# Optimization experiments

Measured on AMD Instinct MI355X. Metric: run time of the kernel, lower is better.

Reference implementation:

```python
import jax, jax.numpy as jnp
import numpy as np

B, CIN, COUT, K, H, W, STYLE_DIM = 16, 128, 128, 3, 128, 128, 512

def setup_inputs() -> dict:
    key = jax.random.key(0)
    k1, k2, k3, k4 = jax.random.split(key, 4)
    x = jax.random.normal(k1, (B, CIN, H, W), dtype=jnp.float32)
    style = jax.random.normal(k2, (B, STYLE_DIM), dtype=jnp.float32)
    weight = jax.random.normal(k3, (COUT, CIN, K, K), dtype=jnp.float32)
    mod_w = jax.random.normal(k4, (CIN, STYLE_DIM), dtype=jnp.float32)
    mod_b = jnp.ones((CIN,), dtype=jnp.float32)  # EqualLinear bias_init=1
    return {"x": x, "style": style, "weight": weight, "mod_w": mod_w, "mod_b": mod_b}

def reference(x, style, weight, mod_w, mod_b):
    b, cin, h, w = x.shape
    cout, _, k, _ = weight.shape
    scale = 1.0 / np.sqrt(cin * k * k)        # conv equalized-lr scale
    lin_scale = 1.0 / np.sqrt(mod_w.shape[1])  # EqualLinear scale (lr_mul=1)
    pad = k // 2
    # affine modulation: EqualLinear(style_dim -> in_channels), bias_init=1
    s = style @ (mod_w * lin_scale).T + mod_b               # [B, Cin]
    # per-sample modulated weights
    wmod = scale * weight[None] * s[:, None, :, None, None]  # [B, Cout, Cin, k, k]
    demod = jax.lax.rsqrt(jnp.sum(wmod * wmod, axis=(2, 3, 4)) + 1e-8)  # [B, Cout]
    wmod = wmod * demod[:, :, None, None, None]
    # grouped conv with groups=batch == vmapped per-sample conv
    def conv_one(xi, wi):
        return jax.lax.conv_general_dilated(
            xi[None], wi, window_strides=(1, 1), padding=[(pad, pad), (pad, pad)],
            dimension_numbers=("NCHW", "OIHW", "NCHW"))[0]
    out = jax.vmap(conv_one)(x, wmod)  # [B, Cout, H, W]
    return out
```

## Files before the change

kernel.cpp:

```cpp
#include <hip/hip_runtime.h>
#include <hip/hip_bf16.h>


typedef __attribute__((ext_vector_type(8))) short short8;
typedef __attribute__((ext_vector_type(4))) float f32x4;

#define XPITCH (130 * 128)
#define CONV_SCALE 0.029462782549439483f
#define LIN_SCALE 0.04419417382415922f

__device__ __forceinline__ void async16(unsigned short* lds, const unsigned short* g) {
  __builtin_amdgcn_global_load_lds((const __attribute__((address_space(1))) void*)g,
                                   (__attribute__((address_space(3))) void*)lds, 16, 0, 0);
}

__device__ __forceinline__ unsigned int pack2bf(float a, float b) {
  unsigned short ha = __builtin_bit_cast(unsigned short, __float2bfloat16(a));
  unsigned short hb = __builtin_bit_cast(unsigned short, __float2bfloat16(b));
  return (unsigned int)ha | ((unsigned int)hb << 16);
}

__global__ void style_kernel(const float* __restrict__ style, const float* __restrict__ mod_w,
                             const float* __restrict__ mod_b, float* __restrict__ s_ws) {
  const int gw = blockIdx.x * 4 + (threadIdx.x >> 6);
  const int b = gw >> 7, cin = gw & 127, lane = threadIdx.x & 63;
  const float4 s0 = *(const float4*)(style + (size_t)b * 512 + lane * 4);
  const float4 s1 = *(const float4*)(style + (size_t)b * 512 + 256 + lane * 4);
  const float4 w0 = *(const float4*)(mod_w + (size_t)cin * 512 + lane * 4);
  const float4 w1 = *(const float4*)(mod_w + (size_t)cin * 512 + 256 + lane * 4);
  float acc = s0.x * w0.x + s0.y * w0.y + s0.z * w0.z + s0.w * w0.w +
              s1.x * w1.x + s1.y * w1.y + s1.z * w1.z + s1.w * w1.w;
#pragma unroll
  for (int off = 32; off; off >>= 1) acc += __shfl_xor(acc, off);
  if (lane == 0) s_ws[b * 128 + cin] = acc * LIN_SCALE + mod_b[cin];
}

__global__ void modw_kernel(const float* __restrict__ weight, const float* __restrict__ s_ws,
                            unsigned short* __restrict__ w_ws) {
  const int bid = blockIdx.x;
  const int b = bid >> 7, cout = bid & 127;
  const int cin = threadIdx.x;
  const float sv = s_ws[b * 128 + cin] * CONV_SCALE;
  const float* wp = weight + ((size_t)cout * 128 + cin) * 9;
  float v[9];
  float ss = 0.f;
#pragma unroll
  for (int j = 0; j < 9; ++j) { v[j] = wp[j] * sv; ss += v[j] * v[j]; }
#pragma unroll
  for (int off = 32; off; off >>= 1) ss += __shfl_down(ss, off);
  __shared__ float red[2];
  if ((threadIdx.x & 63) == 0) red[threadIdx.x >> 6] = ss;
  __syncthreads();
  const float dem = rsqrtf(red[0] + red[1] + 1e-8f);
#pragma unroll
  for (int j = 0; j < 9; ++j) {
    __hip_bfloat16 h = __float2bfloat16(v[j] * dem);
    w_ws[(((size_t)b * 9 + j) * 128 + cout) * 128 + cin] =
        __builtin_bit_cast(unsigned short, h);
  }
}

__global__ __launch_bounds__(256) void nhwc_kernel(const float* __restrict__ x,
                                                   unsigned short* __restrict__ xp) {
  const int b = blockIdx.y, row = blockIdx.x;
  const int tid = threadIdx.x;
  unsigned short* ob = xp + ((size_t)b * 130 + row) * XPITCH;
  if (row == 0 || row == 129) {
    const uint4 z = {0u, 0u, 0u, 0u};
    for (int v = tid; v < 1040; v += 256) ((uint4*)ob)[v] = z;
    return;
  }
  const int y = row - 1;
  __shared__ unsigned short T[128 * 128];
  const float* xb = x + (size_t)b * (128 * 16384) + y * 128;

  const int xc4 = tid & 31;
  const int cing = tid >> 5;
#pragma unroll
  for (int r = 0; r < 4; ++r) {
    const int cin0 = r * 32 + cing * 4;
    const int g = cin0 >> 2;
    float4 f[4];
#pragma unroll
    for (int j = 0; j < 4; ++j)
      f[j] = *(const float4*)(xb + (size_t)(cin0 + j) * 16384 + xc4 * 4);
#pragma unroll
    for (int i = 0; i < 4; ++i) {
      const int xc = xc4 * 4 + i;
      const int gp = g ^ (xc & 31);
      uint2 col;
      col.x = pack2bf(((const float*)&f[0])[i], ((const float*)&f[1])[i]);
      col.y = pack2bf(((const float*)&f[2])[i], ((const float*)&f[3])[i]);
      *(uint2*)(&T[xc * 128 + gp * 4]) = col;
    }
  }
  __syncthreads();
#pragma unroll
  for (int rr = 0; rr < 8; ++rr) {
    const int v = rr * 256 + tid;
    const int cg = v & 15;
    const int xc = v >> 4;
    const int s5 = xc & 31;
    const int g0 = (cg * 2) ^ s5, g1 = (cg * 2 + 1) ^ s5;
    const uint2 a = *(const uint2*)(&T[xc * 128 + g0 * 4]);
    const uint2 c = *(const uint2*)(&T[xc * 128 + g1 * 4]);
    uint4 o;
    o.x = a.x; o.y = a.y; o.z = c.x; o.w = c.y;
    *(uint4*)(ob + (xc + 1) * 128 + cg * 8) = o;
  }
  const uint4 z = {0u, 0u, 0u, 0u};
  if (tid < 16) *(uint4*)(ob + tid * 8) = z;
  else if (tid < 32) *(uint4*)(ob + 129 * 128 + (tid - 16) * 8) = z;
}

__global__ __launch_bounds__(512, 2) void conv_kernel(const unsigned short* __restrict__ xp,
                                                      const unsigned short* __restrict__ wws,
                                                      float* __restrict__ out) {
  __shared__ unsigned short lA[2][128 * 64];
  __shared__ unsigned short lB[2][256 * 64];

  const int tid = threadIdx.x;
  const int bid = (blockIdx.x & 7) * 128 + (blockIdx.x >> 3);
  const int b = bid >> 6, y0 = (bid & 63) * 2;
  const int lane = tid & 63, w = tid >> 6;
  const int wm = w & 1, wn = w >> 1;
  const int l15 = lane & 15, q = lane >> 4;

  f32x4 acc[4][4];
#pragma unroll
  for (int i = 0; i < 4; ++i)
#pragma unroll
    for (int t = 0; t < 4; ++t) acc[i][t] = (f32x4){0.f, 0.f, 0.f, 0.f};

  const unsigned short* xpb = xp + (size_t)b * 130 * XPITCH;
  const unsigned short* wb = wws + (size_t)b * 9 * 128 * 128;

  const int am = tid >> 3;
  const unsigned short* asrc = wb + am * 128 + (((tid & 7) ^ (am & 7)) << 3);
  const unsigned short* bsrc[4];
#pragma unroll
  for (int p = 0; p < 4; ++p) {
    const int g = p * 512 + tid, n = g >> 3;
    const int c16 = (g & 7) ^ (n & 7);
    bsrc[p] = xpb + (size_t)(y0 + (n >> 7)) * XPITCH + (n & 127) * 128 + (c16 << 3);
  }
  const int dst8 = tid * 8;

#define STAGE_STEP(cur_, j3_, ky_, kx_, c0_)                         \
  do {                                                               \
    const int ka = (j3_) * 16384 + (c0_);                            \
    async16(lA[cur_] + dst8, asrc + ka);                             \
    async16(lA[cur_] + 4096 + dst8, asrc + ka + 8192);               \
    const int kb = (ky_)*XPITCH + (kx_)*128 + (c0_);                 \
    async16(lB[cur_] + dst8, bsrc[0] + kb);                          \
    async16(lB[cur_] + 4096 + dst8, bsrc[1] + kb);                   \
    async16(lB[cur_] + 8192 + dst8, bsrc[2] + kb);                   \
    async16(lB[cur_] + 12288 + dst8, bsrc[3] + kb);                  \
  } while (0)

  STAGE_STEP(0, 0, 0, 0, 0);

#pragma unroll
  for (int t = 0; t < 18; ++t) {
    const int cur = t & 1;
    if (t < 17) {
      const int tn = t + 1;
      const int j3n = tn >> 1, c0n = (tn & 1) << 6;
      const int kyn = j3n / 3, kxn = j3n % 3;
      STAGE_STEP(cur ^ 1, j3n, kyn, kxn, c0n);
      asm volatile("s_waitcnt vmcnt(6)" ::: "memory");
    } else {
      asm volatile("s_waitcnt vmcnt(0)" ::: "memory");
    }
    asm volatile("s_barrier" ::: "memory");

    short8 af[2][4], bf[2][4];
#pragma unroll
    for (int s = 0; s < 2; ++s) {
      const int axor = (((s * 4 + q) ^ (l15 & 7)) << 3);
#pragma unroll
      for (int i = 0; i < 4; ++i)
        af[s][i] = *(const short8*)(&lA[cur][(wm * 64 + i * 16 + l15) * 64 + axor]);
#pragma unroll
      for (int i = 0; i < 4; ++i)
        bf[s][i] = *(const short8*)(&lB[cur][(wn * 64 + i * 16 + l15) * 64 + axor]);
    }
    asm volatile("s_waitcnt lgkmcnt(0)" ::: "memory");
    __builtin_amdgcn_sched_barrier(0);
    __builtin_amdgcn_s_setprio(1);
#pragma unroll
    for (int s = 0; s < 2; ++s)
#pragma unroll
      for (int i = 0; i < 4; ++i)
#pragma unroll
        for (int u = 0; u < 4; ++u)
          acc[i][u] = __builtin_amdgcn_mfma_f32_16x16x32_bf16(af[s][i], bf[s][u], acc[i][u], 0, 0, 0);
    __builtin_amdgcn_s_setprio(0);
    asm volatile("s_barrier" ::: "memory");
  }
#undef STAGE_STEP

  float* obase = out + (size_t)b * (128 * 16384) + (y0 + (wn >> 1)) * 128 + (wn & 1) * 64;
#pragma unroll
  for (int i = 0; i < 4; ++i) {
    const int coutb = wm * 64 + i * 16 + q * 4;
#pragma unroll
    for (int rr = 0; rr < 4; ++rr) {
      float* orow = obase + (size_t)(coutb + rr) * 16384;
#pragma unroll
      for (int t = 0; t < 4; ++t) orow[t * 16 + l15] = acc[i][t][rr];
    }
  }
}

extern "C" void kernel_launch(void* const* d_in, const int* in_sizes, int n_in,
                              void* d_out, int out_size, void* d_ws, size_t ws_size,
                              hipStream_t stream) {
  const float* x = (const float*)d_in[0];
  const float* style = (const float*)d_in[1];
  const float* weight = (const float*)d_in[2];
  const float* mod_w = (const float*)d_in[3];
  const float* mod_b = (const float*)d_in[4];
  float* out = (float*)d_out;

  char* ws = (char*)d_ws;
  float* s_ws = (float*)ws;
  unsigned short* w_ws = (unsigned short*)(ws + 8192);
  unsigned short* xp = (unsigned short*)(ws + (5u << 20));

  style_kernel<<<512, 256, 0, stream>>>(style, mod_w, mod_b, s_ws);
  modw_kernel<<<16 * 128, 128, 0, stream>>>(weight, s_ws, w_ws);
  nhwc_kernel<<<dim3(130, 16), 256, 0, stream>>>(x, xp);
  conv_kernel<<<16 * 64, 512, 0, stream>>>(xp, w_ws, out);
}
```

Before: 348.1 us.

## Fold style modulation into input and demod into output epilogue; triple-buffer conv

Instead of building a modulated bf16 weight tensor per sample, the style scale is applied to the input during the NHWC bf16 conversion. A single shared bf16 weight tensor is used by all samples, and demodulation is computed from precomputed squared weight sums and applied as a per-output-channel scale in the conv epilogue. This removes the per-batch weight generation and makes weight loads shared across blocks, which is friendlier to L2. The conv main loop is also restructured into 36 smaller K-steps of 32 channels with a three-stage LDS pipeline. Rounding behaviour changes because bf16 quantisation now happens on the modulated activations rather than on the modulated weights.

```diff
diff --git a/kernel.cpp b/kernel.cpp
--- a/kernel.cpp
+++ b/kernel.cpp
@@ -35,32 +35,35 @@
   if (lane == 0) s_ws[b * 128 + cin] = acc * LIN_SCALE + mod_b[cin];
 }
 
-__global__ void modw_kernel(const float* __restrict__ weight, const float* __restrict__ s_ws,
-                            unsigned short* __restrict__ w_ws) {
-  const int bid = blockIdx.x;
-  const int b = bid >> 7, cout = bid & 127;
-  const int cin = threadIdx.x;
-  const float sv = s_ws[b * 128 + cin] * CONV_SCALE;
+__global__ void wprep_kernel(const float* __restrict__ weight,
+                             unsigned short* __restrict__ wsh, float* __restrict__ W2) {
+  const int cout = blockIdx.x, cin = threadIdx.x;
   const float* wp = weight + ((size_t)cout * 128 + cin) * 9;
-  float v[9];
   float ss = 0.f;
 #pragma unroll
-  for (int j = 0; j < 9; ++j) { v[j] = wp[j] * sv; ss += v[j] * v[j]; }
-#pragma unroll
-  for (int off = 32; off; off >>= 1) ss += __shfl_down(ss, off);
-  __shared__ float red[2];
-  if ((threadIdx.x & 63) == 0) red[threadIdx.x >> 6] = ss;
-  __syncthreads();
-  const float dem = rsqrtf(red[0] + red[1] + 1e-8f);
-#pragma unroll
   for (int j = 0; j < 9; ++j) {
-    __hip_bfloat16 h = __float2bfloat16(v[j] * dem);
-    w_ws[(((size_t)b * 9 + j) * 128 + cout) * 128 + cin] =
-        __builtin_bit_cast(unsigned short, h);
-  }
+    const float v = wp[j] * CONV_SCALE;
+    ss += v * v;
+    wsh[j * 16384 + cout * 128 + cin] =
+        __builtin_bit_cast(unsigned short, __float2bfloat16(v));
+  }
+  W2[cout * 128 + cin] = ss;
+}
+
+__global__ void demod_kernel(const float* __restrict__ W2, const float* __restrict__ s_ws,
+                             float* __restrict__ d_ws) {
+  const int gw = blockIdx.x * 4 + (threadIdx.x >> 6);
+  const int b = gw >> 7, cout = gw & 127, lane = threadIdx.x & 63;
+  const float2 w2 = *(const float2*)(W2 + cout * 128 + lane * 2);
+  const float2 sv = *(const float2*)(s_ws + b * 128 + lane * 2);
+  float acc = w2.x * sv.x * sv.x + w2.y * sv.y * sv.y;
+#pragma unroll
+  for (int off = 32; off; off >>= 1) acc += __shfl_xor(acc, off);
+  if (lane == 0) d_ws[b * 128 + cout] = rsqrtf(acc + 1e-8f);
 }
 
 __global__ __launch_bounds__(256) void nhwc_kernel(const float* __restrict__ x,
+                                                   const float* __restrict__ s_ws,
                                                    unsigned short* __restrict__ xp) {
   const int b = blockIdx.y, row = blockIdx.x;
   const int tid = threadIdx.x;
@@ -80,10 +83,14 @@
   for (int r = 0; r < 4; ++r) {
     const int cin0 = r * 32 + cing * 4;
     const int g = cin0 >> 2;
+    const float4 sv = *(const float4*)(s_ws + b * 128 + cin0);
     float4 f[4];
 #pragma unroll
-    for (int j = 0; j < 4; ++j)
+    for (int j = 0; j < 4; ++j) {
       f[j] = *(const float4*)(xb + (size_t)(cin0 + j) * 16384 + xc4 * 4);
+      const float s = ((const float*)&sv)[j];
+      f[j].x *= s; f[j].y *= s; f[j].z *= s; f[j].w *= s;
+    }
 #pragma unroll
     for (int i = 0; i < 4; ++i) {
       const int xc = xc4 * 4 + i;
@@ -114,10 +121,11 @@
 }
 
 __global__ __launch_bounds__(512, 2) void conv_kernel(const unsigned short* __restrict__ xp,
-                                                      const unsigned short* __restrict__ wws,
+                                                      const unsigned short* __restrict__ wsh,
+                                                      const float* __restrict__ d_ws,
                                                       float* __restrict__ out) {
-  __shared__ unsigned short lA[2][128 * 64];
-  __shared__ unsigned short lB[2][256 * 64];
+  __shared__ unsigned short lA[3][4096];
+  __shared__ unsigned short lB[3][8192];
 
   const int tid = threadIdx.x;
   const int bid = (blockIdx.x & 7) * 128 + (blockIdx.x >> 3);
@@ -133,72 +141,74 @@
     for (int t = 0; t < 4; ++t) acc[i][t] = (f32x4){0.f, 0.f, 0.f, 0.f};
 
   const unsigned short* xpb = xp + (size_t)b * 130 * XPITCH;
-  const unsigned short* wb = wws + (size_t)b * 9 * 128 * 128;
-
-  const int am = tid >> 3;
-  const unsigned short* asrc = wb + am * 128 + (((tid & 7) ^ (am & 7)) << 3);
-  const unsigned short* bsrc[4];
-#pragma unroll
-  for (int p = 0; p < 4; ++p) {
-    const int g = p * 512 + tid, n = g >> 3;
-    const int c16 = (g & 7) ^ (n & 7);
-    bsrc[p] = xpb + (size_t)(y0 + (n >> 7)) * XPITCH + (n & 127) * 128 + (c16 << 3);
+
+  const int ar = tid >> 3, ap = tid & 7;
+  const int alog = ap ^ (ar & 7);
+  const unsigned short* asrc = wsh + (ar * 2 + (alog >> 2)) * 128 + (alog & 3) * 8;
+  const unsigned short* bsrc[2];
+#pragma unroll
+  for (int p = 0; p < 2; ++p) {
+    const int c = p * 512 + tid;
+    const int r = c >> 3, ph = c & 7, lg = ph ^ (r & 7);
+    const int n = r * 2 + (lg >> 2), kq = lg & 3;
+    bsrc[p] = xpb + (size_t)(y0 + (n >> 7)) * XPITCH + (n & 127) * 128 + kq * 8;
   }
   const int dst8 = tid * 8;
 
-#define STAGE_STEP(cur_, j3_, ky_, kx_, c0_)                         \
-  do {                                                               \
-    const int ka = (j3_) * 16384 + (c0_);                            \
-    async16(lA[cur_] + dst8, asrc + ka);                             \
-    async16(lA[cur_] + 4096 + dst8, asrc + ka + 8192);               \
-    const int kb = (ky_)*XPITCH + (kx_)*128 + (c0_);                 \
-    async16(lB[cur_] + dst8, bsrc[0] + kb);                          \
-    async16(lB[cur_] + 4096 + dst8, bsrc[1] + kb);                   \
-    async16(lB[cur_] + 8192 + dst8, bsrc[2] + kb);                   \
-    async16(lB[cur_] + 12288 + dst8, bsrc[3] + kb);                  \
+  const int phys = (((l15 & 1) << 2) | q) ^ (l15 >> 1);
+  const int aoff = (wm * 32 + (l15 >> 1)) * 64 + phys * 8;
+  const int boff = (wn * 32 + (l15 >> 1)) * 64 + phys * 8;
+
+#define STAGE(buf_, tap_, ky_, kx_, c0_)                              \
+  do {                                                                \
+    async16(lA[buf_] + dst8, asrc + (tap_) * 16384 + (c0_));          \
+    const int kb_ = (ky_)*XPITCH + (kx_)*128 + (c0_);                 \
+    async16(lB[buf_] + dst8, bsrc[0] + kb_);                          \
+    async16(lB[buf_] + 4096 + dst8, bsrc[1] + kb_);                   \
   } while (0)
 
-  STAGE_STEP(0, 0, 0, 0, 0);
-
-#pragma unroll
-  for (int t = 0; t < 18; ++t) {
-    const int cur = t & 1;
-    if (t < 17) {
-      const int tn = t + 1;
-      const int j3n = tn >> 1, c0n = (tn & 1) << 6;
-      const int kyn = j3n / 3, kxn = j3n % 3;
-      STAGE_STEP(cur ^ 1, j3n, kyn, kxn, c0n);
+  STAGE(0, 0, 0, 0, 0);
+  STAGE(1, 0, 0, 0, 32);
+
+#pragma unroll
+  for (int t = 0; t < 36; ++t) {
+    const int cur = t % 3;
+    if (t < 34) {
+      const int tn = t + 2, tap = tn >> 2, c0 = (tn & 3) * 32;
+      const int ky = tap / 3, kx = tap % 3;
+      STAGE((tn) % 3, tap, ky, kx, c0);
       asm volatile("s_waitcnt vmcnt(6)" ::: "memory");
+    } else if (t == 34) {
+      asm volatile("s_waitcnt vmcnt(3)" ::: "memory");
     } else {
       asm volatile("s_waitcnt vmcnt(0)" ::: "memory");
     }
     asm volatile("s_barrier" ::: "memory");
 
-    short8 af[2][4], bf[2][4];
-#pragma unroll
-    for (int s = 0; s < 2; ++s) {
-      const int axor = (((s * 4 + q) ^ (l15 & 7)) << 3);
-#pragma unroll
-      for (int i = 0; i < 4; ++i)
-        af[s][i] = *(const short8*)(&lA[cur][(wm * 64 + i * 16 + l15) * 64 + axor]);
-#pragma unroll
-      for (int i = 0; i < 4; ++i)
-        bf[s][i] = *(const short8*)(&lB[cur][(wn * 64 + i * 16 + l15) * 64 + axor]);
-    }
+    short8 af[4], bf[4];
+#pragma unroll
+    for (int i = 0; i < 4; ++i) af[i] = *(const short8*)(&lA[cur][aoff + i * 512]);
+#pragma unroll
+    for (int u = 0; u < 4; ++u) bf[u] = *(const short8*)(&lB[cur][boff + u * 512]);
     asm volatile("s_waitcnt lgkmcnt(0)" ::: "memory");
     __builtin_amdgcn_sched_barrier(0);
     __builtin_amdgcn_s_setprio(1);
 #pragma unroll
-    for (int s = 0; s < 2; ++s)
-#pragma unroll
-      for (int i = 0; i < 4; ++i)
-#pragma unroll
-        for (int u = 0; u < 4; ++u)
-          acc[i][u] = __builtin_amdgcn_mfma_f32_16x16x32_bf16(af[s][i], bf[s][u], acc[i][u], 0, 0, 0);
+    for (int i = 0; i < 4; ++i)
+#pragma unroll
+      for (int u = 0; u < 4; ++u)
+        acc[i][u] = __builtin_amdgcn_mfma_f32_16x16x32_bf16(af[i], bf[u], acc[i][u], 0, 0, 0);
     __builtin_amdgcn_s_setprio(0);
-    asm volatile("s_barrier" ::: "memory");
-  }
-#undef STAGE_STEP
+    if (t < 35) asm volatile("s_barrier" ::: "memory");
+  }
+#undef STAGE
+
+  float dmv[4][4];
+#pragma unroll
+  for (int i = 0; i < 4; ++i)
+#pragma unroll
+    for (int rr = 0; rr < 4; ++rr)
+      dmv[i][rr] = d_ws[b * 128 + wm * 64 + i * 16 + q * 4 + rr];
 
   float* obase = out + (size_t)b * (128 * 16384) + (y0 + (wn >> 1)) * 128 + (wn & 1) * 64;
 #pragma unroll
@@ -208,7 +218,7 @@
     for (int rr = 0; rr < 4; ++rr) {
       float* orow = obase + (size_t)(coutb + rr) * 16384;
 #pragma unroll
-      for (int t = 0; t < 4; ++t) orow[t * 16 + l15] = acc[i][t][rr];
+      for (int t = 0; t < 4; ++t) orow[t * 16 + l15] = acc[i][t][rr] * dmv[i][rr];
     }
   }
 }
@@ -225,11 +235,14 @@
 
   char* ws = (char*)d_ws;
   float* s_ws = (float*)ws;
-  unsigned short* w_ws = (unsigned short*)(ws + 8192);
-  unsigned short* xp = (unsigned short*)(ws + (5u << 20));
+  float* d_dm = (float*)(ws + 8192);
+  float* W2 = (float*)(ws + 16384);
+  unsigned short* wsh = (unsigned short*)(ws + 81920);
+  unsigned short* xp = (unsigned short*)(ws + (1u << 20));
 
   style_kernel<<<512, 256, 0, stream>>>(style, mod_w, mod_b, s_ws);
-  modw_kernel<<<16 * 128, 128, 0, stream>>>(weight, s_ws, w_ws);
-  nhwc_kernel<<<dim3(130, 16), 256, 0, stream>>>(x, xp);
-  conv_kernel<<<16 * 64, 512, 0, stream>>>(xp, w_ws, out);
-}
+  wprep_kernel<<<128, 128, 0, stream>>>(weight, wsh, W2);
+  nhwc_kernel<<<dim3(130, 16), 256, 0, stream>>>(x, s_ws, xp);
+  demod_kernel<<<512, 256, 0, stream>>>(W2, s_ws, d_dm);
+  conv_kernel<<<16 * 64, 512, 0, stream>>>(xp, wsh, d_dm, out);
+}
```

New measurement: 329.8 us. 1.06x faster.
